# Kernel optimization log

Measured on AMD Instinct MI355X. Metric: run time of the kernel, lower is better.

Reference implementation:

```python
import jax, jax.numpy as jnp
import numpy as np

H = 128  # LSTM hidden size


def lstm_layer(x, Wih, Whh, bih, bhh):
    # x: [B, T, Fin]; Wih: [4H, Fin]; Whh: [4H, H]; biases: [4H]
    xg = jnp.einsum('btf,gf->btg', x, Wih) + bih  # precompute input gates [B,T,4H]
    B = x.shape[0]
    h0 = jnp.zeros((B, H), x.dtype)
    c0 = jnp.zeros((B, H), x.dtype)

    def step(carry, xt):
        h, c = carry
        g = xt + h @ Whh.T + bhh  # [B,4H]
        i, f, gg, o = jnp.split(g, 4, axis=-1)  # torch gate order: i,f,g,o
        i = jax.nn.sigmoid(i)
        f = jax.nn.sigmoid(f)
        gg = jnp.tanh(gg)
        o = jax.nn.sigmoid(o)
        c = f * c + i * gg
        h = o * jnp.tanh(c)
        return (h, c), h

    (hT, cT), hs = jax.lax.scan(step, (h0, c0), jnp.swapaxes(xg, 0, 1))
    return jnp.swapaxes(hs, 0, 1), hT  # all-step outputs [B,T,H], final h [B,H]


def setup_inputs() -> dict:
    key = jax.random.key(0)
    ks = jax.random.split(key, 20)
    B, T, F = 512, 912, 32
    s = 1.0 / np.sqrt(H)  # torch LSTM/Linear init scale
    u = lambda k, shape: jax.random.uniform(k, shape, jnp.float32, -s, s)
    return {
        'x': jax.random.normal(ks[0], (B, T, F), jnp.float32),
        'Wih0': u(ks[1], (4 * H, F)),
        'Whh0': u(ks[2], (4 * H, H)),
        'bih0': u(ks[3], (4 * H,)),
        'bhh0': u(ks[4], (4 * H,)),
        'Wih123': u(ks[5], (3, 4 * H, H)),
        'Whh123': u(ks[6], (3, 4 * H, H)),
        'bih123': u(ks[7], (3, 4 * H)),
        'bhh123': u(ks[8], (3, 4 * H)),
        'Wopt': u(ks[9], (4, H)), 'bopt': u(ks[10], (4,)),
        'Wlot': u(ks[11], (4, H)), 'blot': u(ks[12], (4,)),
        'Wtp': u(ks[13], (4, H)), 'btp': u(ks[14], (4,)),
        'Wsl': u(ks[15], (4, H)), 'bsl': u(ks[16], (4,)),
    }


def reference(x, Wih0, Whh0, bih0, bhh0, Wih123, Whh123, bih123, bhh123,
              Wopt, bopt, Wlot, blot, Wtp, btp, Wsl, bsl):
    out, h0f = lstm_layer(x, Wih0, Whh0, bih0, bhh0)
    finals = [h0f]
    for l in range(3):  # fixed small layer loop
        out, hf = lstm_layer(out, Wih123[l], Whh123[l], bih123[l], bhh123[l])
        finals.append(hf)
    hN = jnp.stack(finals)  # h_n: [4, B, H] (final hidden per layer, as torch returns)
    # heads: Sequential applies softmax/sigmoid once, forward applies it again
    opt = jax.nn.softmax(jax.nn.softmax(hN @ Wopt.T + bopt, axis=-1), axis=-1)
    lot = jax.nn.sigmoid(jax.nn.sigmoid(hN @ Wlot.T + blot))
    tp = jax.nn.sigmoid(jax.nn.sigmoid(hN @ Wtp.T + btp))
    sl = jax.nn.sigmoid(jax.nn.sigmoid(hN @ Wsl.T + bsl))
    return (opt, tp, sl, lot)
```

## Files before the change

### kernel.cpp

```cpp
#include <hip/hip_runtime.h>

#define DEV __device__ __forceinline__

typedef __attribute__((ext_vector_type(8))) short short8;
typedef __attribute__((ext_vector_type(4))) float floatx4;
typedef unsigned long long ull;

static constexpr int B_ = 512, T_ = 912, H_ = 128, F_ = 32;
static constexpr int RING = 64;
static constexpr size_t HN_OFF   = 1024;
static constexpr size_t XT_OFF   = HN_OFF + (size_t)4 * 512 * 128 * 2;
static constexpr size_t RING_OFF = XT_OFF + (size_t)T_ * B_ * F_ * 2;
static constexpr size_t RING_QW_PER_GRP = (size_t)RING * 16 * 128 / 4;

DEV unsigned short bf16rne(float f) {
    unsigned u = __builtin_bit_cast(unsigned, f);
    u += 0x7FFFu + ((u >> 16) & 1u);
    return (unsigned short)(u >> 16);
}
DEV float bf16tof(unsigned short u) {
    return __builtin_bit_cast(float, ((unsigned)u) << 16);
}
DEV float sigm(float x) {
    return __builtin_amdgcn_rcpf(1.f + __builtin_amdgcn_exp2f(-1.44269504f * x));
}
DEV float tanh_(float x) {
    return 2.f * __builtin_amdgcn_rcpf(1.f + __builtin_amdgcn_exp2f(-2.88539008f * x)) - 1.f;
}

__global__ __launch_bounds__(256) void xpose(const float* __restrict__ x,
                                             unsigned short* __restrict__ xT) {
    int tid = blockIdx.x * 256 + threadIdx.x;
    if (tid >= B_ * T_ * 4) return;
    int k = tid & 3;
    int r = tid >> 2;
    int b = r / T_;
    int t = r - b * T_;
    const float* p = x + ((size_t)r * 32 + k * 8);
    short8 v;
#pragma unroll
    for (int j = 0; j < 8; j++) v[j] = (short)bf16rne(p[j]);
    *(short8*)(xT + ((size_t)t * 512 + b) * 32 + k * 8) = v;
}

__global__ __launch_bounds__(512, 2) void lstm_scan(
    const float* __restrict__ Wih0, const float* __restrict__ Whh0,
    const float* __restrict__ bih0, const float* __restrict__ bhh0,
    const float* __restrict__ Wih123, const float* __restrict__ Whh123,
    const float* __restrict__ bih123, const float* __restrict__ bhh123,
    char* __restrict__ ws) {
    const int tid  = threadIdx.x;
    const int wv   = tid >> 6;
    const int lane = tid & 63;
    const int col  = lane & 15;
    const int quad = lane >> 4;
    const int blk  = blockIdx.x;
    const int layer = blk >> 5;
    const int grp   = blk & 31;
    const int b0    = grp * 16;

    unsigned* flags = (unsigned*)ws;
    unsigned* cons  = (unsigned*)(ws + 512);
    unsigned short* hN = (unsigned short*)(ws + HN_OFF);
    const unsigned short* xT = (const unsigned short*)(ws + XT_OFF);
    ull* ringAll = (ull*)(ws + RING_OFF);

    __shared__ unsigned short Ah[2][16][136];
    __shared__ unsigned short Xl[2][16][136];

    for (int i = tid; i < 16 * 136; i += 512) ((unsigned short*)Ah[0])[i] = 0;

    short8 wh[4][4];
    short8 wx[4][4];
    float  bias_q[4];
    const int KX = (layer == 0) ? 1 : 4;
    {
        const float *Wih, *Whh, *bih, *bhh;
        int kin;
        if (layer == 0) { Wih = Wih0; Whh = Whh0; bih = bih0; bhh = bhh0; kin = 32; }
        else {
            Wih = Wih123 + (size_t)(layer - 1) * 512 * 128;
            Whh = Whh123 + (size_t)(layer - 1) * 512 * 128;
            bih = bih123 + (size_t)(layer - 1) * 512;
            bhh = bhh123 + (size_t)(layer - 1) * 512;
            kin = 128;
        }
#pragma unroll
        for (int q = 0; q < 4; q++) {
            int row = q * 128 + wv * 16 + col;
            bias_q[q] = bih[row] + bhh[row];
#pragma unroll
            for (int kt = 0; kt < 4; kt++) {
                const float* ph = Whh + (size_t)row * 128 + kt * 32 + quad * 8;
                short8 v;
#pragma unroll
                for (int j = 0; j < 8; j++) v[j] = (short)bf16rne(ph[j]);
                wh[kt][q] = v;
            }
        }
#pragma unroll
        for (int q = 0; q < 4; q++) {
            int row = q * 128 + wv * 16 + col;
#pragma unroll
            for (int kt = 0; kt < 4; kt++) {
                const float* ph = Whh + (size_t)row * 128 + kt * 32 + quad * 8;
                short8 v;
#pragma unroll
                for (int j = 0; j < 8; j++) v[j] = (short)bf16rne(ph[j]);
                wh[q][kt] = v;
            }
#pragma unroll
            for (int kt = 0; kt < 4; kt++) {
                short8 v = {0, 0, 0, 0, 0, 0, 0, 0};
                if (kt < KX) {
                    const float* px = Wih + (size_t)row * kin + kt * 32 + quad * 8;
#pragma unroll
                    for (int j = 0; j < 8; j++) v[j] = (short)bf16rne(px[j]);
                }
                wx[q][kt] = v;
            }
        }
    }

    unsigned* myflag   = &flags[layer * 32 + grp];
    unsigned* prevflag = &flags[(layer > 0 ? layer - 1 : 0) * 32 + grp];
    unsigned* mycons   = &cons[(layer > 0 ? layer - 1 : 0) * 32 + grp];
    unsigned* nextcons = &cons[layer * 32 + grp];
    ull* prodRing = ringAll + ((size_t)layer * 32 + grp) * RING_QW_PER_GRP;
    ull* consRing = ringAll + ((size_t)(layer > 0 ? layer - 1 : 0) * 32 + grp) * RING_QW_PER_GRP;

    const int cb = tid >> 5;
    const int ck = tid & 31;

    if (layer > 0) {
        if (tid == 0) {
            while (__hip_atomic_load(prevflag, __ATOMIC_RELAXED, __HIP_MEMORY_SCOPE_AGENT) < 2u) {}
        }
        __syncthreads();
        ull d0 = __hip_atomic_load(consRing + (size_t)cb * 32 + ck,
                                   __ATOMIC_RELAXED, __HIP_MEMORY_SCOPE_AGENT);
        *(ull*)&Xl[0][cb][ck * 4] = d0;
    }
    short8 axc = {0, 0, 0, 0, 0, 0, 0, 0};
    if (layer == 0)
        axc = *(const short8*)(xT + ((size_t)0 * 512 + b0 + col) * 32 + quad * 8);
    __syncthreads();

    float c4[4] = {0.f, 0.f, 0.f, 0.f};
    const int hcol = wv * 16 + col;

    for (int t = 0; t < T_; ++t) {
        const int rb = t & 1;
        if (tid == 0 && layer > 0)
            __hip_atomic_store(mycons, (unsigned)(t + 1), __ATOMIC_RELAXED, __HIP_MEMORY_SCOPE_AGENT);
        unsigned pf = 0xffffffffu, pc = 0xffffffffu;
        if (tid == 0) {
            if (layer > 0 && t + 2 < T_)
                pf = __hip_atomic_load(prevflag, __ATOMIC_RELAXED, __HIP_MEMORY_SCOPE_AGENT);
            if (layer < 3 && t >= 64)
                pc = __hip_atomic_load(nextcons, __ATOMIC_RELAXED, __HIP_MEMORY_SCOPE_AGENT);
        }
        if (layer < 3 && t > 0) {
            ull hv = *(const ull*)&Ah[rb][cb][ck * 4];
            __hip_atomic_store(prodRing + (size_t)((t - 1) & (RING - 1)) * 512 + cb * 32 + ck,
                               hv, __ATOMIC_RELAXED, __HIP_MEMORY_SCOPE_AGENT);
        }
        ull dn = 0;
        if (layer > 0 && t + 1 < T_)
            dn = __hip_atomic_load(consRing + (size_t)((t + 1) & (RING - 1)) * 512 + cb * 32 + ck,
                                   __ATOMIC_RELAXED, __HIP_MEMORY_SCOPE_AGENT);
        short8 axn = {0, 0, 0, 0, 0, 0, 0, 0};
        if (layer == 0 && t + 1 < T_)
            axn = *(const short8*)(xT + ((size_t)(t + 1) * 512 + b0 + col) * 32 + quad * 8);

        short8 ah[4];
        {
            const unsigned short* base = &Ah[rb][col][quad * 8];
#pragma unroll
            for (int kt = 0; kt < 4; kt++) ah[kt] = *(const short8*)(base + kt * 32);
        }
        short8 axf[4];
        if (layer > 0) {
            const unsigned short* base = &Xl[rb][col][quad * 8];
#pragma unroll
            for (int kt = 0; kt < 4; kt++) axf[kt] = *(const short8*)(base + kt * 32);
        }
        floatx4 acc[4];
#pragma unroll
        for (int q = 0; q < 4; q++) {
            float bq = bias_q[q];
            floatx4 a = {bq, bq, bq, bq};
            acc[q] = a;
        }
#pragma unroll
        for (int kt = 0; kt < 4; kt++)
#pragma unroll
            for (int q = 0; q < 4; q++)
                acc[q] = __builtin_amdgcn_mfma_f32_16x16x32_bf16(ah[kt], wh[q][kt], acc[q], 0, 0, 0);
        if (layer == 0) {
#pragma unroll
            for (int q = 0; q < 4; q++)
                acc[q] = __builtin_amdgcn_mfma_f32_16x16x32_bf16(axc, wx[q][0], acc[q], 0, 0, 0);
        } else {
#pragma unroll
            for (int kt = 0; kt < 4; kt++)
#pragma unroll
                for (int q = 0; q < 4; q++)
                    acc[q] = __builtin_amdgcn_mfma_f32_16x16x32_bf16(axf[kt], wx[q][kt], acc[q], 0, 0, 0);
        }
#pragma unroll
        for (int r = 0; r < 4; r++) {
            float iv = sigm(acc[0][r]);
            float fv = sigm(acc[1][r]);
            float gv = tanh_(acc[2][r]);
            float ov = sigm(acc[3][r]);
            float cv = fv * c4[r] + iv * gv;
            c4[r] = cv;
            float hv = ov * tanh_(cv);
            unsigned short hb = bf16rne(hv);
            int m = quad * 4 + r;
            Ah[1 - rb][m][hcol] = hb;
            if (t == T_ - 1)
                hN[((size_t)layer * 512 + b0 + m) * 128 + hcol] = hb;
        }
        if (layer > 0 && t + 1 < T_)
            *(ull*)&Xl[1 - rb][cb][ck * 4] = dn;
        if (tid == 0) {
            if (layer > 0 && t + 2 < T_) {
                unsigned tgt = (unsigned)(t + 3);
                if (pf < tgt)
                    while (__hip_atomic_load(prevflag, __ATOMIC_RELAXED, __HIP_MEMORY_SCOPE_AGENT) < tgt) {}
            }
            if (layer < 3 && t >= 64) {
                unsigned tgt = (unsigned)(t - 63);
                if (pc < tgt)
                    while (__hip_atomic_load(nextcons, __ATOMIC_RELAXED, __HIP_MEMORY_SCOPE_AGENT) < tgt) {}
            }
        }
        __syncthreads();
        if (tid == 0 && layer < 3)
            __hip_atomic_store(myflag, (unsigned)t, __ATOMIC_RELAXED, __HIP_MEMORY_SCOPE_AGENT);
        if (layer == 0) axc = axn;
    }
    if (layer < 3) {
        ull hv = *(const ull*)&Ah[0][cb][ck * 4];
        __hip_atomic_store(prodRing + (size_t)(911 & (RING - 1)) * 512 + cb * 32 + ck,
                           hv, __ATOMIC_RELAXED, __HIP_MEMORY_SCOPE_AGENT);
        __syncthreads();
        if (tid == 0)
            __hip_atomic_store(myflag, 912u, __ATOMIC_RELAXED, __HIP_MEMORY_SCOPE_AGENT);
    }
}

__global__ __launch_bounds__(256) void heads(
    const unsigned short* __restrict__ hN,
    const float* __restrict__ Wopt, const float* __restrict__ bopt,
    const float* __restrict__ Wlot, const float* __restrict__ blot,
    const float* __restrict__ Wtp,  const float* __restrict__ btp,
    const float* __restrict__ Wsl,  const float* __restrict__ bsl,
    float* __restrict__ out) {
    int tid = blockIdx.x * 256 + threadIdx.x;
    if (tid >= 4 * 4 * 512) return;
    int b  = tid & 511;
    int l  = (tid >> 9) & 3;
    int hd = tid >> 11;
    const float *W, *bb;
    if      (hd == 0) { W = Wopt; bb = bopt; }
    else if (hd == 1) { W = Wtp;  bb = btp;  }
    else if (hd == 2) { W = Wsl;  bb = bsl;  }
    else              { W = Wlot; bb = blot; }
    const unsigned short* h = hN + ((size_t)l * 512 + b) * 128;
    float z0 = bb[0], z1 = bb[1], z2 = bb[2], z3 = bb[3];
    for (int i = 0; i < 128; i++) {
        float hv = bf16tof(h[i]);
        z0 += hv * W[0 * 128 + i];
        z1 += hv * W[1 * 128 + i];
        z2 += hv * W[2 * 128 + i];
        z3 += hv * W[3 * 128 + i];
    }
    float o0, o1, o2, o3;
    if (hd == 0) {
        float m = fmaxf(fmaxf(z0, z1), fmaxf(z2, z3));
        float e0 = __builtin_amdgcn_exp2f((z0 - m) * 1.44269504f);
        float e1 = __builtin_amdgcn_exp2f((z1 - m) * 1.44269504f);
        float e2 = __builtin_amdgcn_exp2f((z2 - m) * 1.44269504f);
        float e3 = __builtin_amdgcn_exp2f((z3 - m) * 1.44269504f);
        float rs = __builtin_amdgcn_rcpf(e0 + e1 + e2 + e3);
        float p0 = e0 * rs, p1 = e1 * rs, p2 = e2 * rs, p3 = e3 * rs;
        float m2 = fmaxf(fmaxf(p0, p1), fmaxf(p2, p3));
        float f0 = __builtin_amdgcn_exp2f((p0 - m2) * 1.44269504f);
        float f1 = __builtin_amdgcn_exp2f((p1 - m2) * 1.44269504f);
        float f2 = __builtin_amdgcn_exp2f((p2 - m2) * 1.44269504f);
        float f3 = __builtin_amdgcn_exp2f((p3 - m2) * 1.44269504f);
        float rs2 = __builtin_amdgcn_rcpf(f0 + f1 + f2 + f3);
        o0 = f0 * rs2; o1 = f1 * rs2; o2 = f2 * rs2; o3 = f3 * rs2;
    } else {
        o0 = sigm(sigm(z0)); o1 = sigm(sigm(z1));
        o2 = sigm(sigm(z2)); o3 = sigm(sigm(z3));
    }
    float* o = out + (size_t)hd * 8192 + ((size_t)l * 512 + b) * 4;
    o[0] = o0; o[1] = o1; o[2] = o2; o[3] = o3;
}

extern "C" void kernel_launch(void* const* d_in, const int* in_sizes, int n_in,
                              void* d_out, int out_size, void* d_ws, size_t ws_size,
                              hipStream_t stream) {
    (void)in_sizes; (void)n_in; (void)out_size; (void)ws_size;
    const float* x      = (const float*)d_in[0];
    const float* Wih0   = (const float*)d_in[1];
    const float* Whh0   = (const float*)d_in[2];
    const float* bih0   = (const float*)d_in[3];
    const float* bhh0   = (const float*)d_in[4];
    const float* Wih123 = (const float*)d_in[5];
    const float* Whh123 = (const float*)d_in[6];
    const float* bih123 = (const float*)d_in[7];
    const float* bhh123 = (const float*)d_in[8];
    const float* Wopt = (const float*)d_in[9];
    const float* bopt = (const float*)d_in[10];
    const float* Wlot = (const float*)d_in[11];
    const float* blot = (const float*)d_in[12];
    const float* Wtp  = (const float*)d_in[13];
    const float* btp  = (const float*)d_in[14];
    const float* Wsl  = (const float*)d_in[15];
    const float* bsl  = (const float*)d_in[16];
    char* ws = (char*)d_ws;

    hipMemsetAsync(ws, 0, 1024, stream);
    xpose<<<(B_ * T_ * 4 + 255) / 256, 256, 0, stream>>>(x, (unsigned short*)(ws + XT_OFF));
    lstm_scan<<<128, 512, 0, stream>>>(Wih0, Whh0, bih0, bhh0,
                                       Wih123, Whh123, bih123, bhh123, ws);
    heads<<<32, 256, 0, stream>>>((const unsigned short*)(ws + HN_OFF),
                                  Wopt, bopt, Wlot, blot, Wtp, btp, Wsl, bsl,
                                  (float*)d_out);
}
```

Before: 2.311 ms.

## Batch inter-layer ring traffic and flag syncs into chunks of eight timesteps

Layer-pipelined LSTM blocks now publish hidden states to the inter-layer ring and poll producer/consumer flags once every eight timesteps instead of every step. A 16-deep LDS history of h lets eight steps be stored in one burst, and consumers prefetch the next eight inputs into registers. This cuts per-step global atomics and spin-wait latency on the serial critical path. In exchange it adds pipeline lag between layers, uses more registers and LDS, and relies on the changed flag units (chunk index) being handled correctly.

```diff
diff --git a/kernel.cpp b/kernel.cpp
--- a/kernel.cpp
+++ b/kernel.cpp
@@ -65,10 +65,10 @@
     const unsigned short* xT = (const unsigned short*)(ws + XT_OFF);
     ull* ringAll = (ull*)(ws + RING_OFF);
 
-    __shared__ unsigned short Ah[2][16][136];
-    __shared__ unsigned short Xl[2][16][136];
-
-    for (int i = tid; i < 16 * 136; i += 512) ((unsigned short*)Ah[0])[i] = 0;
+    __shared__ unsigned short Ah[16][16][132];
+    __shared__ unsigned short Xl[2][16][132];
+
+    for (int i = tid; i < 16 * 16 * 132; i += 512) ((unsigned short*)Ah)[i] = 0;
 
     short8 wh[4][4];
     short8 wx[4][4];
@@ -95,18 +95,6 @@
                 short8 v;
 #pragma unroll
                 for (int j = 0; j < 8; j++) v[j] = (short)bf16rne(ph[j]);
-                wh[kt][q] = v;
-            }
-        }
-#pragma unroll
-        for (int q = 0; q < 4; q++) {
-            int row = q * 128 + wv * 16 + col;
-#pragma unroll
-            for (int kt = 0; kt < 4; kt++) {
-                const float* ph = Whh + (size_t)row * 128 + kt * 32 + quad * 8;
-                short8 v;
-#pragma unroll
-                for (int j = 0; j < 8; j++) v[j] = (short)bf16rne(ph[j]);
                 wh[q][kt] = v;
             }
 #pragma unroll
@@ -132,14 +120,20 @@
     const int cb = tid >> 5;
     const int ck = tid & 31;
 
+    ull dcur[8], dnext[8];
+#pragma unroll
+    for (int i = 0; i < 8; i++) { dcur[i] = 0; dnext[i] = 0; }
+
     if (layer > 0) {
         if (tid == 0) {
             while (__hip_atomic_load(prevflag, __ATOMIC_RELAXED, __HIP_MEMORY_SCOPE_AGENT) < 2u) {}
         }
         __syncthreads();
-        ull d0 = __hip_atomic_load(consRing + (size_t)cb * 32 + ck,
-                                   __ATOMIC_RELAXED, __HIP_MEMORY_SCOPE_AGENT);
-        *(ull*)&Xl[0][cb][ck * 4] = d0;
+#pragma unroll
+        for (int i = 0; i < 8; i++)
+            dcur[i] = __hip_atomic_load(consRing + (size_t)i * 512 + cb * 32 + ck,
+                                        __ATOMIC_RELAXED, __HIP_MEMORY_SCOPE_AGENT);
+        *(ull*)&Xl[0][cb][ck * 4] = dcur[0];
     }
     short8 axc = {0, 0, 0, 0, 0, 0, 0, 0};
     if (layer == 0)
@@ -150,38 +144,48 @@
     const int hcol = wv * 16 + col;
 
     for (int t = 0; t < T_; ++t) {
-        const int rb = t & 1;
-        if (tid == 0 && layer > 0)
-            __hip_atomic_store(mycons, (unsigned)(t + 1), __ATOMIC_RELAXED, __HIP_MEMORY_SCOPE_AGENT);
+        const int j = t & 7;
         unsigned pf = 0xffffffffu, pc = 0xffffffffu;
-        if (tid == 0) {
-            if (layer > 0 && t + 2 < T_)
-                pf = __hip_atomic_load(prevflag, __ATOMIC_RELAXED, __HIP_MEMORY_SCOPE_AGENT);
-            if (layer < 3 && t >= 64)
-                pc = __hip_atomic_load(nextcons, __ATOMIC_RELAXED, __HIP_MEMORY_SCOPE_AGENT);
-        }
-        if (layer < 3 && t > 0) {
-            ull hv = *(const ull*)&Ah[rb][cb][ck * 4];
-            __hip_atomic_store(prodRing + (size_t)((t - 1) & (RING - 1)) * 512 + cb * 32 + ck,
-                               hv, __ATOMIC_RELAXED, __HIP_MEMORY_SCOPE_AGENT);
-        }
-        ull dn = 0;
-        if (layer > 0 && t + 1 < T_)
-            dn = __hip_atomic_load(consRing + (size_t)((t + 1) & (RING - 1)) * 512 + cb * 32 + ck,
-                                   __ATOMIC_RELAXED, __HIP_MEMORY_SCOPE_AGENT);
+        if (j == 0) {
+            if (tid == 0) {
+                if (layer > 0)
+                    __hip_atomic_store(mycons, (unsigned)(t >> 3), __ATOMIC_RELAXED,
+                                       __HIP_MEMORY_SCOPE_AGENT);
+                if (layer > 0 && t + 16 < T_)
+                    pf = __hip_atomic_load(prevflag, __ATOMIC_RELAXED, __HIP_MEMORY_SCOPE_AGENT);
+                if (layer < 3 && t >= 64)
+                    pc = __hip_atomic_load(nextcons, __ATOMIC_RELAXED, __HIP_MEMORY_SCOPE_AGENT);
+            }
+            if (layer < 3 && t >= 8) {
+#pragma unroll
+                for (int i = 0; i < 8; i++) {
+                    int s = t - 8 + i;
+                    ull hv = *(const ull*)&Ah[s & 15][cb][ck * 4];
+                    __hip_atomic_store(prodRing + (size_t)(s & (RING - 1)) * 512 + cb * 32 + ck,
+                                       hv, __ATOMIC_RELAXED, __HIP_MEMORY_SCOPE_AGENT);
+                }
+            }
+            if (layer > 0 && t + 8 < T_) {
+#pragma unroll
+                for (int i = 0; i < 8; i++)
+                    dnext[i] = __hip_atomic_load(consRing + (size_t)((t + 8 + i) & (RING - 1)) * 512
+                                                 + cb * 32 + ck,
+                                                 __ATOMIC_RELAXED, __HIP_MEMORY_SCOPE_AGENT);
+            }
+        }
         short8 axn = {0, 0, 0, 0, 0, 0, 0, 0};
         if (layer == 0 && t + 1 < T_)
             axn = *(const short8*)(xT + ((size_t)(t + 1) * 512 + b0 + col) * 32 + quad * 8);
 
         short8 ah[4];
         {
-            const unsigned short* base = &Ah[rb][col][quad * 8];
+            const unsigned short* base = &Ah[(t + 15) & 15][col][quad * 8];
 #pragma unroll
             for (int kt = 0; kt < 4; kt++) ah[kt] = *(const short8*)(base + kt * 32);
         }
         short8 axf[4];
         if (layer > 0) {
-            const unsigned short* base = &Xl[rb][col][quad * 8];
+            const unsigned short* base = &Xl[t & 1][col][quad * 8];
 #pragma unroll
             for (int kt = 0; kt < 4; kt++) axf[kt] = *(const short8*)(base + kt * 32);
         }
@@ -219,36 +223,47 @@
             float hv = ov * tanh_(cv);
             unsigned short hb = bf16rne(hv);
             int m = quad * 4 + r;
-            Ah[1 - rb][m][hcol] = hb;
+            Ah[t & 15][m][hcol] = hb;
             if (t == T_ - 1)
                 hN[((size_t)layer * 512 + b0 + m) * 128 + hcol] = hb;
         }
-        if (layer > 0 && t + 1 < T_)
-            *(ull*)&Xl[1 - rb][cb][ck * 4] = dn;
-        if (tid == 0) {
-            if (layer > 0 && t + 2 < T_) {
-                unsigned tgt = (unsigned)(t + 3);
+        if (layer > 0 && t + 1 < T_) {
+            ull stage = (j < 7) ? dcur[j + 1] : dnext[0];
+            *(ull*)&Xl[1 - (t & 1)][cb][ck * 4] = stage;
+        }
+        if (j == 7) {
+#pragma unroll
+            for (int i = 0; i < 8; i++) dcur[i] = dnext[i];
+        }
+        if (j == 7 && tid == 0) {
+            if (layer > 0 && t + 16 < T_) {
+                unsigned tgt = (unsigned)((t >> 3) + 3);
                 if (pf < tgt)
                     while (__hip_atomic_load(prevflag, __ATOMIC_RELAXED, __HIP_MEMORY_SCOPE_AGENT) < tgt) {}
             }
-            if (layer < 3 && t >= 64) {
-                unsigned tgt = (unsigned)(t - 63);
+            if (layer < 3 && t >= 71) {
+                unsigned tgt = (unsigned)(((t + 1) >> 3) - 8);
                 if (pc < tgt)
                     while (__hip_atomic_load(nextcons, __ATOMIC_RELAXED, __HIP_MEMORY_SCOPE_AGENT) < tgt) {}
             }
         }
         __syncthreads();
-        if (tid == 0 && layer < 3)
-            __hip_atomic_store(myflag, (unsigned)t, __ATOMIC_RELAXED, __HIP_MEMORY_SCOPE_AGENT);
+        if (tid == 0 && layer < 3 && t >= 8 && j == 0)
+            __hip_atomic_store(myflag, (unsigned)(t >> 3), __ATOMIC_RELAXED,
+                               __HIP_MEMORY_SCOPE_AGENT);
         if (layer == 0) axc = axn;
     }
     if (layer < 3) {
-        ull hv = *(const ull*)&Ah[0][cb][ck * 4];
-        __hip_atomic_store(prodRing + (size_t)(911 & (RING - 1)) * 512 + cb * 32 + ck,
-                           hv, __ATOMIC_RELAXED, __HIP_MEMORY_SCOPE_AGENT);
+#pragma unroll
+        for (int i = 0; i < 8; i++) {
+            int s = 904 + i;
+            ull hv = *(const ull*)&Ah[s & 15][cb][ck * 4];
+            __hip_atomic_store(prodRing + (size_t)(s & (RING - 1)) * 512 + cb * 32 + ck,
+                               hv, __ATOMIC_RELAXED, __HIP_MEMORY_SCOPE_AGENT);
+        }
         __syncthreads();
         if (tid == 0)
-            __hip_atomic_store(myflag, 912u, __ATOMIC_RELAXED, __HIP_MEMORY_SCOPE_AGENT);
+            __hip_atomic_store(myflag, 200u, __ATOMIC_RELAXED, __HIP_MEMORY_SCOPE_AGENT);
     }
 }
 
```

Result: slower. 2.579 ms (+11.6%).
